# Performance work log

Measured on AMD Instinct MI355X. Metric: run time of the kernel, lower is better.

## Reference

```python
import jax, jax.numpy as jnp
import numpy as np

B, N, F, K, H = 2, 1024, 64, 8, 4
M1 = K + 1                # 9
M2 = (F - 1) * K + 1      # 505
TEMP = 1.0


def setup_inputs() -> dict:
    key = jax.random.key(0)
    ks = jax.random.split(key, 8)
    x = jax.random.normal(ks[0], (B, N, F), dtype=jnp.float32)
    # Bernoulli(0.05) dense adjacency
    adj = (jax.random.uniform(ks[1], (B, N, N)) < 0.05).astype(jnp.float32)
    mask = jnp.ones((B, N), dtype=jnp.float32)
    Wl = jax.random.normal(ks[2], (F, K * H), dtype=jnp.float32) * 0.05
    bl = jnp.zeros((K * H,), dtype=jnp.float32)
    Wr = jax.random.normal(ks[3], (F, K * H), dtype=jnp.float32) * 0.05
    br = jnp.zeros((K * H,), dtype=jnp.float32)
    # fixed affine layer: y = x @ aff_w + aff_b, aff_w[:, :F] = -I, aff_b[M2] = 1
    aff_w = jnp.zeros((F, M1 * M2), dtype=jnp.float32).at[:, :F].set(-jnp.eye(F, dtype=jnp.float32))
    aff_b = jnp.zeros((M1 * M2,), dtype=jnp.float32).at[M2].set(1.0)
    Wm = jax.random.normal(ks[4], (M1 * M2, F), dtype=jnp.float32) * 0.02
    bm = jnp.zeros((F,), dtype=jnp.float32)
    return dict(x=x, adj=adj, mask=mask, Wl=Wl, bl=bl, Wr=Wr, br=br,
                aff_w=aff_w, aff_b=aff_b, Wm=Wm, bm=bm)


def reference(x, adj, mask, Wl, bl, Wr, br, aff_w, aff_b, Wm, bm):
    # --- multi-head edge attention ---
    x_l = (x @ Wl + bl).reshape(B, N, K, H)   # [B,N,K,H]
    x_r = (x @ Wr + br).reshape(B, N, K, H)
    # scores[b,i,j,n,g] = leaky_relu(x_l[b,j] + x_r[b,i]) / temp
    scores = jax.nn.leaky_relu(x_l[:, None, :, :, :] + x_r[:, :, None, :, :]) / TEMP  # [B,N,N,K,H]
    attn_mask = mask[:, None, :] * mask[:, :, None]                # [B,N,N]
    scores = jnp.where(attn_mask[..., None, None] == 0, -1e9, scores)
    att = jax.nn.softmax(scores, axis=2)                           # softmax over source nodes j
    att = jnp.maximum(att * adj[..., None, None], 1e-6)            # clamp(min=1e-6) STE trick
    att = att / jnp.sum(att, axis=2, keepdims=True)                # renormalize
    # --- attention-weighted neighbor gather ---
    x_h = x.reshape(B, N, H, F // H)
    agg = jnp.einsum('bjgk,bijng->bingk', x_h, att).reshape(B, N, K, F)  # [B,N,K,F]
    # --- fixed affine + FFT log-domain geometric mean ---
    x_aff = (agg @ aff_w + aff_b).reshape(B, N, K, M1, M2)
    x_fft = jnp.fft.fft2(x_aff)                                    # over (M1,M2)
    mag = jnp.exp(jnp.mean(jnp.log(jnp.abs(x_fft) + 1e-6), axis=2))  # [B,N,M1,M2]
    ang = jnp.sum(jnp.angle(x_fft), axis=2)
    x_agg = jnp.fft.ifft2(mag * jnp.exp(1j * ang)).real.reshape(B, N, M1 * M2)
    # --- output MLP + node mask ---
    out = x_agg @ Wm + bm
    return out * mask[..., None]
```

## Files before the change

kernel.cpp:

```cpp
#include <hip/hip_runtime.h>
#include <math.h>

#define NN 1024
#define FD 64
#define CH 32
#define M1D 9
#define M2D 505
#define QH 253
#define THALF 2273
#define KPAD 4608
#define KSPLIT 16
#define KCHUNK 288
#define G1SZ 291456
#define G1KS 8

#define FSQRT(x) __builtin_amdgcn_sqrtf(x)
#define FRCP(x)  __builtin_amdgcn_rcpf(x)

typedef short short8 __attribute__((ext_vector_type(8)));
typedef float f32x4 __attribute__((ext_vector_type(4)));

__device__ __forceinline__ unsigned short f2bf(float x) {
    unsigned int u = __builtin_bit_cast(unsigned int, x);
    return (unsigned short)((u + 0x7FFFu + ((u >> 16) & 1u)) >> 16);
}

__device__ __forceinline__ void cvt8_3(const float* v, uint4& h4, uint4& m4, uint4& l4) {
    unsigned short h[8], m[8], l[8];
    #pragma unroll
    for (int i = 0; i < 8; i++) {
        unsigned short hh = f2bf(v[i]);
        float hf = __builtin_bit_cast(float, (unsigned int)hh << 16);
        float r1 = v[i] - hf;
        unsigned short mm = f2bf(r1);
        float mf = __builtin_bit_cast(float, (unsigned int)mm << 16);
        h[i] = hh; m[i] = mm;
        l[i] = f2bf(r1 - mf);
    }
    h4 = make_uint4((unsigned)h[0] | ((unsigned)h[1] << 16), (unsigned)h[2] | ((unsigned)h[3] << 16),
                    (unsigned)h[4] | ((unsigned)h[5] << 16), (unsigned)h[6] | ((unsigned)h[7] << 16));
    m4 = make_uint4((unsigned)m[0] | ((unsigned)m[1] << 16), (unsigned)m[2] | ((unsigned)m[3] << 16),
                    (unsigned)m[4] | ((unsigned)m[5] << 16), (unsigned)m[6] | ((unsigned)m[7] << 16));
    l4 = make_uint4((unsigned)l[0] | ((unsigned)l[1] << 16), (unsigned)l[2] | ((unsigned)l[3] << 16),
                    (unsigned)l[4] | ((unsigned)l[5] << 16), (unsigned)l[6] | ((unsigned)l[7] << 16));
}

#define SAH 0
#define SAM 2560
#define SAL 5120
#define SBH 7680
#define SBM 10240
#define SBL 12800

#define OFF_SUMXP 1024
#define OFF_GMT   4096
#define OFF_XL    151552
#define OFF_XR    217088
#define OFF_AGG   282624
#define OFF_Y     1331200
#define OFF_G1P   6049792
#define OFF_WT    8381440

__global__ __launch_bounds__(256) void fused_pre_kernel(
    const float* __restrict__ x,
    const float* __restrict__ Wl, const float* __restrict__ bl,
    const float* __restrict__ Wr, const float* __restrict__ br,
    const float* __restrict__ Wm, const float* __restrict__ bm,
    const float* __restrict__ mask,
    float* __restrict__ xl, float* __restrict__ xr,
    float* __restrict__ sumxp, float* __restrict__ G1p,
    float* __restrict__ Wt, float* __restrict__ out)
{
    __shared__ __align__(16) unsigned char pool[30720];
    int bid = blockIdx.x, tid = threadIdx.x;

    if (bid < 576) {
        int mt = bid & 7, m1 = (bid >> 3) % 9, ks = bid / 72;
        int r0 = mt * 64, k0 = ks * 64;
        const float* Wmb = Wm + (size_t)m1 * M2D * FD;
        unsigned short* Sp = (unsigned short*)pool;
        int r = tid >> 2, kg = (tid & 3) * 8;
        int rr = r0 + r;
        uint4 Ah[2], Am[2], Al[2], Bh[2], Bm[2], Bl[2];
        #pragma unroll
        for (int c = 0; c < 2; c++) {
            float va[8], vb[8];
            #pragma unroll
            for (int j = 0; j < 8; j++) {
                int m2 = k0 + c*32 + kg + j;
                float v = 0.f;
                if (rr < 506 && m2 < M2D) {
                    int q = rr >> 1;
                    int t = (q * m2) % M2D;
                    float ang = (float)t * (-6.2831853f / 505.0f);
                    float s, cc; __sincosf(ang, &s, &cc);
                    v = (rr & 1) ? -s : cc;
                }
                va[j] = v;
                vb[j] = (m2 < M2D) ? Wmb[(size_t)m2*FD + r] : 0.f;
            }
            cvt8_3(va, Ah[c], Am[c], Al[c]);
            cvt8_3(vb, Bh[c], Bm[c], Bl[c]);
        }
        int w = tid >> 6, lane = tid & 63, lm = lane & 15, quad = lane >> 4;
        f32x4 acc0 = {0.f,0.f,0.f,0.f}, acc1 = acc0, acc2 = acc0, acc3 = acc0;
        #pragma unroll
        for (int c = 0; c < 2; c++) {
            if (c) __syncthreads();
            *(uint4*)&Sp[SAH + r*40 + kg] = Ah[c];
            *(uint4*)&Sp[SAM + r*40 + kg] = Am[c];
            *(uint4*)&Sp[SAL + r*40 + kg] = Al[c];
            *(uint4*)&Sp[SBH + r*40 + kg] = Bh[c];
            *(uint4*)&Sp[SBM + r*40 + kg] = Bm[c];
            *(uint4*)&Sp[SBL + r*40 + kg] = Bl[c];
            __syncthreads();
            int bo = (w*16 + lm)*40 + quad*8;
            short8 bfh = *(const short8*)&Sp[SBH + bo];
            short8 bfm = *(const short8*)&Sp[SBM + bo];
            short8 bfl = *(const short8*)&Sp[SBL + bo];
            #pragma unroll
            for (int t = 0; t < 4; t++) {
                int ao = (t*16 + lm)*40 + quad*8;
                short8 ah = *(const short8*)&Sp[SAH + ao];
                short8 am = *(const short8*)&Sp[SAM + ao];
                short8 al = *(const short8*)&Sp[SAL + ao];
                f32x4 a = (t==0)?acc0:(t==1)?acc1:(t==2)?acc2:acc3;
                a = __builtin_amdgcn_mfma_f32_16x16x32_bf16(ah, bfh, a, 0, 0, 0);
                a = __builtin_amdgcn_mfma_f32_16x16x32_bf16(am, bfh, a, 0, 0, 0);
                a = __builtin_amdgcn_mfma_f32_16x16x32_bf16(ah, bfm, a, 0, 0, 0);
                a = __builtin_amdgcn_mfma_f32_16x16x32_bf16(am, bfm, a, 0, 0, 0);
                a = __builtin_amdgcn_mfma_f32_16x16x32_bf16(al, bfh, a, 0, 0, 0);
                a = __builtin_amdgcn_mfma_f32_16x16x32_bf16(ah, bfl, a, 0, 0, 0);
                if (t==0) acc0 = a; else if (t==1) acc1 = a; else if (t==2) acc2 = a; else acc3 = a;
            }
        }
        float* G1k = G1p + (size_t)ks * G1SZ;
        int f = w*16 + lm;
        #pragma unroll
        for (int t = 0; t < 4; t++) {
            f32x4 a = (t==0)?acc0:(t==1)?acc1:(t==2)?acc2:acc3;
            #pragma unroll
            for (int i = 0; i < 4; i++) {
                int m = t*16 + quad*4 + i;
                int rg = r0 + m;
                if (rg >= 506) continue;
                int q = rg >> 1, reim = rg & 1;
                G1k[(size_t)(m1*QH + q)*128 + reim*64 + f] = a[i];
            }
        }
    } else if (bid < 1088) {
        int grp = tid >> 6, lt = tid & 63;
        int node = (bid - 576)*4 + grp;
        float* xrow = (float*)pool + grp*FD;
        xrow[lt] = x[(size_t)node*FD + lt];
        __syncthreads();
        int c = lt & 31;
        const float* W = (lt < 32) ? Wl : Wr;
        float acc = (lt < 32) ? bl[c] : br[c];
        #pragma unroll
        for (int f = 0; f < FD; f++) acc += xrow[f] * W[f*CH + c];
        float* dst = (lt < 32) ? xl : xr;
        dst[(size_t)node*CH + c] = acc;
    } else if (bid < 1096) {
        int bb = (bid - 1088)*4 + (tid >> 6);
        int f = tid & 63;
        int b = bb >> 4, chunk = bb & 15;
        const float* xb = x + (size_t)b * NN * FD;
        float acc = 0.f;
        int j0 = chunk * 64;
        #pragma unroll 4
        for (int j = j0; j < j0 + 64; j++) acc += xb[j*FD + f];
        sumxp[bb*64 + f] = acc;
    } else if (bid < 1224) {
        int idx = (bid - 1096)*256 + tid;
        float4 bv = ((const float4*)bm)[idx & 15];
        float mk = mask[idx >> 4];
        bv.x *= mk; bv.y *= mk; bv.z *= mk; bv.w *= mk;
        ((float4*)out)[idx] = bv;
    } else {
        int idx = (bid - 1224)*256 + tid;
        int m = idx >> 9, col = idx & 511;
        float v = 0.f;
        if (col < 506) {
            int q = col >> 1;
            int t = (q * m) % M2D;
            float ang = (float)t * (-6.2831853f / 505.0f);
            float s, c; __sincosf(ang, &s, &c);
            v = (col & 1) ? s : c;
        }
        Wt[idx] = v;
    }
}

__global__ __launch_bounds__(256) void fused_mid_kernel(
    const float* __restrict__ x, const float* __restrict__ adj,
    const float* __restrict__ xl, const float* __restrict__ xr,
    const float* __restrict__ sumxp, const float* __restrict__ G1p,
    float* __restrict__ agg, unsigned short* __restrict__ GmT)
{
    int bid = blockIdx.x, tid = threadIdx.x;

    if (bid >= 2048) {
        int bid2 = bid - 2048;
        if (bid2 == 64) {
            for (int i = tid; i < 31*64; i += 256) {
                int t = THALF + (i >> 6), f = i & 63;
                *(unsigned int*)&GmT[(size_t)f*KPAD + 2*t] = 0u;
            }
            return;
        }
        __shared__ float wps[18];
        if (tid < 9) {
            float s, c; __sincosf((float)tid * (-6.2831853f / 9.0f), &s, &c);
            wps[2*tid] = c; wps[2*tid+1] = s;
        }
        __syncthreads();
        int qq = bid2*4 + (tid >> 6);
        int f = tid & 63;
        if (qq >= QH) return;
        float ar[M1D], ai[M1D];
        #pragma unroll
        for (int m1 = 0; m1 < M1D; m1++) {
            size_t o = (size_t)(m1*QH + qq) * 128 + f;
            float sr = 0.f, si = 0.f;
            #pragma unroll
            for (int ks = 0; ks < G1KS; ks++) {
                sr += G1p[(size_t)ks*G1SZ + o];
                si += G1p[(size_t)ks*G1SZ + o + 64];
            }
            ar[m1] = sr; ai[m1] = si;
        }
        #pragma unroll
        for (int p = 0; p < 5; p++) {
            {
                int t = (p == 0) ? qq : (QH + (p-1)*M2D + qq);
                float gr = 0.f, gi = 0.f;
                #pragma unroll
                for (int m1 = 0; m1 < M1D; m1++) {
                    int pm = (p * m1) % M1D;
                    float cr = wps[2*pm], ci = -wps[2*pm+1];
                    gr += ar[m1]*cr - ai[m1]*ci;
                    gi += ar[m1]*ci + ai[m1]*cr;
                }
                float scale = (t == 0) ? (1.0f/4545.0f) : (2.0f/4545.0f);
                unsigned int pk = (unsigned int)f2bf(gr*scale) | ((unsigned int)f2bf(-gi*scale) << 16);
                *(unsigned int*)&GmT[(size_t)f*KPAD + 2*t] = pk;
            }
            if (p >= 1 && qq >= 1) {
                int t = QH + (p-1)*M2D + (M2D - qq);
                float gr = 0.f, gi = 0.f;
                #pragma unroll
                for (int m1 = 0; m1 < M1D; m1++) {
                    int pm = (p * m1) % M1D;
                    float cr = wps[2*pm], ci = -wps[2*pm+1];
                    float aim = -ai[m1];
                    gr += ar[m1]*cr - aim*ci;
                    gi += ar[m1]*ci + aim*cr;
                }
                float scale = 2.0f/4545.0f;
                unsigned int pk = (unsigned int)f2bf(gr*scale) | ((unsigned int)f2bf(-gi*scale) << 16);
                *(unsigned int*)&GmT[(size_t)f*KPAD + 2*t] = pk;
            }
        }
        return;
    }

    int node = bid;
    int b = node >> 10;
    __shared__ float xr_s[CH], Zinv[CH], Sinv[CH];
    __shared__ float red16[16][CH];
    __shared__ int act_list[NN + 8];
    __shared__ int act_n;
    __shared__ float qv2[64][CH];

    if (tid < CH) xr_s[tid] = xr[(size_t)node*CH + tid];
    if (tid == 0) act_n = 0;
    __syncthreads();

    int c = tid & 31, jl = tid >> 5;
    const float* xlb = xl + ((size_t)b << 10) * CH;
    const float* adjrow = adj + (size_t)node * NN;

    int c2 = tid & 15, jl16 = tid >> 4;
    const float2* xlb2 = (const float2*)xlb;
    float xrcx = xr_s[2*c2], xrcy = xr_s[2*c2+1];
    float zx = 0.f, zy = 0.f;
    for (int j0 = jl16; j0 < NN; j0 += 128) {
        float2 sv[8];
        #pragma unroll
        for (int u = 0; u < 8; u++) sv[u] = xlb2[(size_t)(j0 + u*16)*16 + c2];
        #pragma unroll
        for (int u = 0; u < 8; u++) {
            float s0 = sv[u].x + xrcx; s0 = s0 > 0.f ? s0 : 0.01f * s0;
            float s1 = sv[u].y + xrcy; s1 = s1 > 0.f ? s1 : 0.01f * s1;
            zx += __expf(s0); zy += __expf(s1);
        }
    }
    red16[jl16][2*c2]   = zx;
    red16[jl16][2*c2+1] = zy;

    float av[4];
    #pragma unroll
    for (int u = 0; u < 4; u++) av[u] = adjrow[tid + u*256];
    __syncthreads();
    if (tid < CH) {
        float z = 0.f;
        #pragma unroll
        for (int r = 0; r < 16; r++) z += red16[r][tid];
        Zinv[tid] = FRCP(z);
    }
    #pragma unroll
    for (int u = 0; u < 4; u++)
        if (av[u] != 0.f) { int p = atomicAdd(&act_n, 1); act_list[p] = tid + u*256; }
    __syncthreads();
    int nact = act_n;

    int f = tid & 63, n0 = tid >> 6;
    int g = f >> 4;
    int c0 = n0*4 + g, c1 = (n0+4)*4 + g;
    const float* xb = x + ((size_t)b << 10) * FD;
    float acc0 = 0.f, acc1 = 0.f, sacc = 0.f;

    for (int base = 0; base < nact; base += 64) {
        int cnt = min(64, nact - base);
        int cntp = (cnt + 7) & ~7;
        for (int u = tid; u < (cnt << 5); u += 256) {
            int jj = u >> 5, cc = u & 31;
            int j = act_list[base + jj];
            float s = xlb[j*CH + cc] + xr_s[cc];
            s = s > 0.f ? s : 0.01f * s;
            float pv = __expf(s) * Zinv[cc];
            float qq = fmaxf(pv, 1e-6f) - 1e-6f;
            qv2[jj][cc] = qq;
            sacc += qq;
        }
        for (int u = tid + (cnt << 5); u < (cntp << 5); u += 256)
            qv2[u >> 5][u & 31] = 0.f;
        if (tid < cntp - cnt) act_list[base + cnt + tid] = act_list[base];
        __syncthreads();
        for (int jb = 0; jb < cntp; jb += 8) {
            float xv[8];
            #pragma unroll
            for (int u = 0; u < 8; u++) xv[u] = xb[act_list[base + jb + u]*FD + f];
            #pragma unroll
            for (int u = 0; u < 8; u++) {
                acc0 += qv2[jb+u][c0] * xv[u];
                acc1 += qv2[jb+u][c1] * xv[u];
            }
        }
        __syncthreads();
    }
    red16[jl][c] = sacc;
    __syncthreads();
    if (tid < CH) {
        float s = 0.f;
        #pragma unroll
        for (int r = 0; r < 8; r++) s += red16[r][tid];
        Sinv[tid] = FRCP(s + (float)NN * 1e-6f);
    }
    __syncthreads();
    float sx = 0.f;
    #pragma unroll
    for (int cchunk = 0; cchunk < 16; cchunk++) sx += sumxp[(b*16 + cchunk)*64 + f];
    sx *= 1e-6f;
    agg[(size_t)node*512 + n0*FD + f]       = (acc0 + sx) * Sinv[c0];
    agg[(size_t)node*512 + (n0+4)*FD + f]   = (acc1 + sx) * Sinv[c1];
}

__global__ __launch_bounds__(256) void ay_kernel(const float* __restrict__ agg,
                                                 const float* __restrict__ Wt,
                                                 unsigned short* __restrict__ Yb) {
    int slab = blockIdx.x, nt = blockIdx.y;
    int tid = threadIdx.x;
    __shared__ float As2[64][68];
    __shared__ float Bs[64][64];
    int tm = (tid >> 4) * 4, tf = (tid & 15) * 4;
    float ra[16], rb[16];
    #pragma unroll
    for (int i = 0; i < 16; i++) {
        int l = tid + i*256;
        int r = l >> 6, k = l & 63;
        ra[i] = agg[(size_t)(slab*64 + r)*64 + k];
    }
    #pragma unroll
    for (int i = 0; i < 16; i++) {
        int l = tid + i*256;
        rb[i] = Wt[(size_t)(l >> 6)*512 + nt*64 + (l & 63)];
    }
    #pragma unroll
    for (int i = 0; i < 16; i++) { int l = tid + i*256; As2[l & 63][l >> 6] = ra[i]; }
    #pragma unroll
    for (int i = 0; i < 16; i++) { int l = tid + i*256; Bs[l >> 6][l & 63] = rb[i]; }
    __syncthreads();
    float acc[4][4] = {{0.f}};
    #pragma unroll 8
    for (int k = 0; k < 64; k++) {
        float4 a = *(const float4*)&As2[k][tm];
        float4 b = *(const float4*)&Bs[k][tf];
        acc[0][0] += a.x*b.x; acc[0][1] += a.x*b.y; acc[0][2] += a.x*b.z; acc[0][3] += a.x*b.w;
        acc[1][0] += a.y*b.x; acc[1][1] += a.y*b.y; acc[1][2] += a.y*b.z; acc[1][3] += a.y*b.w;
        acc[2][0] += a.z*b.x; acc[2][1] += a.z*b.y; acc[2][2] += a.z*b.z; acc[2][3] += a.z*b.w;
        acc[3][0] += a.w*b.x; acc[3][1] += a.w*b.y; acc[3][2] += a.w*b.z; acc[3][3] += a.w*b.w;
    }
    __syncthreads();
    #pragma unroll
    for (int i = 0; i < 4; i++)
        #pragma unroll
        for (int j = 0; j < 4; j++)
            As2[tm + i][tf + j] = acc[i][j];
    __syncthreads();

    int qloc = tid & 31, node = tid >> 5;
    unsigned short* Yrow = Yb + (size_t)(slab*8 + node)*KPAD;
    int q = nt*32 + qloc;

    if (q <= 252) {
        float2 Av[8];
        #pragma unroll
        for (int n = 0; n < 8; n++)
            Av[n] = make_float2(As2[node*8 + n][2*qloc], As2[node*8 + n][2*qloc + 1]);

        const float CPt[5] = {1.0f, 0.766044443119f, 0.173648177667f, -0.5f, -0.939692620786f};
        const float SPt[5] = {0.0f, -0.642787609687f, -0.984807753012f, -0.866025403784f, -0.342020143326f};

        #define Y_PROD(CSIGN, TIDX)                                            \
        {                                                                      \
            float Pr = 1.f, Pi = 0.f, rp2 = 1.f;                               \
            _Pragma("unroll")                                                  \
            for (int n = 0; n < 8; n++) {                                      \
                float Xr = cp - Av[n].x, Xi = sp - (CSIGN) * Av[n].y;          \
                rp2 *= (Xr*Xr + Xi*Xi);                                        \
                float nPr = Pr*Xr - Pi*Xi;                                     \
                Pi = Pr*Xi + Pi*Xr; Pr = nPr;                                  \
            }                                                                  \
            float pAbs = FSQRT(Pr*Pr + Pi*Pi);                                 \
            float rp8 = FSQRT(FSQRT(FSQRT(FSQRT(rp2))));                       \
            float s = rp8 * FRCP(fmaxf(pAbs, 1e-20f));                         \
            unsigned int pk = (unsigned int)f2bf(s*Pr) | ((unsigned int)f2bf(s*Pi) << 16); \
            *(unsigned int*)&Yrow[2*(TIDX)] = pk;                              \
        }

        #pragma unroll
        for (int p = 0; p < 5; p++) {
            float cp = CPt[p], sp = SPt[p];
            int tfwd = (p == 0) ? q : (QH + (p-1)*M2D + q);
            Y_PROD(1.f, tfwd);
            if (p >= 1 && q >= 1) {
                int tmir = QH + (p-1)*M2D + (M2D - q);
                Y_PROD(-1.f, tmir);
            }
        }
        #undef Y_PROD
    }
    if (nt == 7 && tid < 248) {
        int rr = tid / 31, cc2 = tid % 31;
        unsigned short* Yr2 = Yb + (size_t)(slab*8 + rr)*KPAD;
        *(unsigned int*)&Yr2[2*THALF + 2*cc2] = 0u;
    }
}

__global__ __launch_bounds__(256) void gemm_kernel(const unsigned short* __restrict__ Yb,
                                                   const unsigned short* __restrict__ GmT,
                                                   const float* __restrict__ mask,
                                                   float* __restrict__ out) {
    int mtile = blockIdx.x, kc = blockIdx.y;
    int tid = threadIdx.x;
    __shared__ unsigned short Ys[64*40];
    __shared__ unsigned short Gs[64*40];
    int m0 = mtile * 64;
    int k0 = kc * KCHUNK;
    int r = tid >> 2, kg = (tid & 3) * 8;
    const unsigned short* Ysrc = Yb + (size_t)(m0 + r)*KPAD + k0 + kg;
    const unsigned short* Gsrc = GmT + (size_t)r*KPAD + k0 + kg;
    uint4 ya = *(const uint4*)Ysrc;
    uint4 ga = *(const uint4*)Gsrc;
    int w = tid >> 6, lane = tid & 63;
    int lm = lane & 15, quad = lane >> 4;
    f32x4 acc0 = {0.f,0.f,0.f,0.f}, acc1 = acc0, acc2 = acc0, acc3 = acc0;
    for (int ks = 0; ks < KCHUNK; ks += 32) {
        *(uint4*)&Ys[r*40 + kg] = ya;
        *(uint4*)&Gs[r*40 + kg] = ga;
        __syncthreads();
        if (ks + 32 < KCHUNK) {
            ya = *(const uint4*)(Ysrc + ks + 32);
            ga = *(const uint4*)(Gsrc + ks + 32);
        }
        short8 b  = *(const short8*)&Gs[(w*16 + lm)*40 + quad*8];
        short8 a0 = *(const short8*)&Ys[(lm)*40      + quad*8];
        short8 a1 = *(const short8*)&Ys[(16 + lm)*40 + quad*8];
        short8 a2 = *(const short8*)&Ys[(32 + lm)*40 + quad*8];
        short8 a3 = *(const short8*)&Ys[(48 + lm)*40 + quad*8];
        acc0 = __builtin_amdgcn_mfma_f32_16x16x32_bf16(a0, b, acc0, 0, 0, 0);
        acc1 = __builtin_amdgcn_mfma_f32_16x16x32_bf16(a1, b, acc1, 0, 0, 0);
        acc2 = __builtin_amdgcn_mfma_f32_16x16x32_bf16(a2, b, acc2, 0, 0, 0);
        acc3 = __builtin_amdgcn_mfma_f32_16x16x32_bf16(a3, b, acc3, 0, 0, 0);
        __syncthreads();
    }
    int col = w*16 + lm;
    #pragma unroll
    for (int rr = 0; rr < 4; rr++) {
        int row = m0 + quad*4 + rr;
        atomicAdd(&out[(size_t)row*FD + col],        acc0[rr] * mask[row]);
        atomicAdd(&out[(size_t)(row+16)*FD + col],   acc1[rr] * mask[row+16]);
        atomicAdd(&out[(size_t)(row+32)*FD + col],   acc2[rr] * mask[row+32]);
        atomicAdd(&out[(size_t)(row+48)*FD + col],   acc3[rr] * mask[row+48]);
    }
}

extern "C" void kernel_launch(void* const* d_in, const int* in_sizes, int n_in,
                              void* d_out, int out_size, void* d_ws, size_t ws_size,
                              hipStream_t stream) {
    const float* x    = (const float*)d_in[0];
    const float* adj  = (const float*)d_in[1];
    const float* mask = (const float*)d_in[2];
    const float* Wl   = (const float*)d_in[3];
    const float* bl   = (const float*)d_in[4];
    const float* Wr   = (const float*)d_in[5];
    const float* br   = (const float*)d_in[6];
    const float* Wm   = (const float*)d_in[9];
    const float* bm   = (const float*)d_in[10];
    float* out = (float*)d_out;
    float* ws  = (float*)d_ws;

    float* sumxp = ws + OFF_SUMXP;
    unsigned short* GmT = (unsigned short*)(ws + OFF_GMT);
    float* xl   = ws + OFF_XL;
    float* xr   = ws + OFF_XR;
    float* agg  = ws + OFF_AGG;
    unsigned short* Yb = (unsigned short*)(ws + OFF_Y);
    float* G1p  = ws + OFF_G1P;
    float* Wt   = ws + OFF_WT;

    hipLaunchKernelGGL(fused_pre_kernel, dim3(1352), dim3(256), 0, stream,
                       x, Wl, bl, Wr, br, Wm, bm, mask, xl, xr, sumxp, G1p, Wt, out);
    hipLaunchKernelGGL(fused_mid_kernel, dim3(2113), dim3(256), 0, stream,
                       x, adj, xl, xr, sumxp, G1p, agg, GmT);
    hipLaunchKernelGGL(ay_kernel, dim3(256, 8), dim3(256), 0, stream, agg, Wt, Yb);
    hipLaunchKernelGGL(gemm_kernel, dim3(32, KSPLIT), dim3(256), 0, stream, Yb, GmT, mask, out);
}
```

Before: 159.7 us.

## Compute softmax normalizers via sorted x_l prefix sums and binary search

Adds 64 blocks to the pre kernel. Each block recomputes x_l for one batch and channel, sorts it with a bitonic sort, and stores prefix sums of exp(v) and exp(0.01 v). The mid kernel then finds each node's softmax normalizer Z with a binary search on -x_r and two exponentials, replacing the dense 1024-term leaky-relu exp reduction per node. This trades O(N) work per node for an O(N log N) pre-pass per channel. It adds a serial-sync-heavy sort block that may lengthen the pre kernel's tail, and prefix sums can lose some accuracy compared with direct summation.

```diff
diff --git a/kernel.cpp b/kernel.cpp
--- a/kernel.cpp
+++ b/kernel.cpp
@@ -13,6 +13,7 @@
 #define KCHUNK 288
 #define G1SZ 291456
 #define G1KS 8
+#define SRTSTR 3096
 
 #define FSQRT(x) __builtin_amdgcn_sqrtf(x)
 #define FRCP(x)  __builtin_amdgcn_rcpf(x)
@@ -60,6 +61,7 @@
 #define OFF_Y     1331200
 #define OFF_G1P   6049792
 #define OFF_WT    8381440
+#define OFF_SRT   8414208
 
 __global__ __launch_bounds__(256) void fused_pre_kernel(
     const float* __restrict__ x,
@@ -69,7 +71,8 @@
     const float* __restrict__ mask,
     float* __restrict__ xl, float* __restrict__ xr,
     float* __restrict__ sumxp, float* __restrict__ G1p,
-    float* __restrict__ Wt, float* __restrict__ out)
+    float* __restrict__ Wt, float* __restrict__ srt,
+    float* __restrict__ out)
 {
     __shared__ __align__(16) unsigned char pool[30720];
     int bid = blockIdx.x, tid = threadIdx.x;
@@ -177,7 +180,7 @@
         float mk = mask[idx >> 4];
         bv.x *= mk; bv.y *= mk; bv.z *= mk; bv.w *= mk;
         ((float4*)out)[idx] = bv;
-    } else {
+    } else if (bid < 1352) {
         int idx = (bid - 1224)*256 + tid;
         int m = idx >> 9, col = idx & 511;
         float v = 0.f;
@@ -189,6 +192,67 @@
             v = (col & 1) ? s : c;
         }
         Wt[idx] = v;
+    } else {
+        int bc = bid - 1352;
+        int b = bc >> 5, c = bc & 31;
+        float* sm  = (float*)pool;
+        float* wl  = (float*)(pool + 4096);
+        float* chL = (float*)(pool + 4352);
+        float* chH = (float*)(pool + 5376);
+        if (tid < 64) wl[tid] = Wl[tid*CH + c];
+        __syncthreads();
+        const float* xb = x + (size_t)b * NN * FD;
+        float bc0 = bl[c];
+        for (int i = tid; i < NN; i += 256) {
+            const float* xrw = xb + (size_t)i * FD;
+            float acc = bc0;
+            #pragma unroll
+            for (int f = 0; f < FD; f++) acc += xrw[f] * wl[f];
+            sm[i] = acc;
+        }
+        __syncthreads();
+        for (int k = 2; k <= 1024; k <<= 1) {
+            for (int j = k >> 1; j > 0; j >>= 1) {
+                for (int i = tid; i < 1024; i += 256) {
+                    int p = i ^ j;
+                    if (p > i) {
+                        float a = sm[i], bvv = sm[p];
+                        bool desc = (i & k) != 0;
+                        if (desc ? (a < bvv) : (a > bvv)) { sm[i] = bvv; sm[p] = a; }
+                    }
+                }
+                __syncthreads();
+            }
+        }
+        float* dstS = srt + (size_t)bc * SRTSTR;
+        for (int i = tid; i < 1024; i += 256) dstS[i] = sm[i];
+        float eL[4], eH[4], sl = 0.f, sh = 0.f;
+        #pragma unroll
+        for (int jj = 0; jj < 4; jj++) {
+            float v = sm[4*tid + jj];
+            eL[jj] = sl; eH[jj] = sh;
+            sl += __expf(0.01f * v);
+            sh += __expf(v);
+        }
+        chL[tid] = sl; chH[tid] = sh;
+        __syncthreads();
+        float vL = sl, vH = sh;
+        for (int off = 1; off < 256; off <<= 1) {
+            float aL = (tid >= off) ? chL[tid-off] : 0.f;
+            float aH = (tid >= off) ? chH[tid-off] : 0.f;
+            __syncthreads();
+            vL += aL; vH += aH;
+            chL[tid] = vL; chH[tid] = vH;
+            __syncthreads();
+        }
+        float baseL = tid ? chL[tid-1] : 0.f;
+        float baseH = tid ? chH[tid-1] : 0.f;
+        #pragma unroll
+        for (int jj = 0; jj < 4; jj++) {
+            dstS[1032 + 4*tid + jj] = baseL + eL[jj];
+            dstS[2064 + 4*tid + jj] = baseH + eH[jj];
+        }
+        if (tid == 255) { dstS[1032 + 1024] = chL[255]; dstS[2064 + 1024] = chH[255]; }
     }
 }
 
@@ -196,6 +260,7 @@
     const float* __restrict__ x, const float* __restrict__ adj,
     const float* __restrict__ xl, const float* __restrict__ xr,
     const float* __restrict__ sumxp, const float* __restrict__ G1p,
+    const float* __restrict__ srt,
     float* __restrict__ agg, unsigned short* __restrict__ GmT)
 {
     int bid = blockIdx.x, tid = threadIdx.x;
@@ -281,33 +346,23 @@
     const float* xlb = xl + ((size_t)b << 10) * CH;
     const float* adjrow = adj + (size_t)node * NN;
 
-    int c2 = tid & 15, jl16 = tid >> 4;
-    const float2* xlb2 = (const float2*)xlb;
-    float xrcx = xr_s[2*c2], xrcy = xr_s[2*c2+1];
-    float zx = 0.f, zy = 0.f;
-    for (int j0 = jl16; j0 < NN; j0 += 128) {
-        float2 sv[8];
-        #pragma unroll
-        for (int u = 0; u < 8; u++) sv[u] = xlb2[(size_t)(j0 + u*16)*16 + c2];
-        #pragma unroll
-        for (int u = 0; u < 8; u++) {
-            float s0 = sv[u].x + xrcx; s0 = s0 > 0.f ? s0 : 0.01f * s0;
-            float s1 = sv[u].y + xrcy; s1 = s1 > 0.f ? s1 : 0.01f * s1;
-            zx += __expf(s0); zy += __expf(s1);
-        }
-    }
-    red16[jl16][2*c2]   = zx;
-    red16[jl16][2*c2+1] = zy;
-
     float av[4];
     #pragma unroll
     for (int u = 0; u < 4; u++) av[u] = adjrow[tid + u*256];
-    __syncthreads();
+
     if (tid < CH) {
-        float z = 0.f;
-        #pragma unroll
-        for (int r = 0; r < 16; r++) z += red16[r][tid];
-        Zinv[tid] = FRCP(z);
+        const float* sb = srt + (size_t)((b << 5) + tid) * SRTSTR;
+        float xrc = xr_s[tid];
+        float thr = -xrc;
+        int lo = 0, hi = 1024;
+        while (lo < hi) {
+            int mid = (lo + hi) >> 1;
+            if (sb[mid] <= thr) lo = mid + 1; else hi = mid;
+        }
+        float SLo = sb[1032 + lo];
+        float SHi = sb[2064 + 1024] - sb[2064 + lo];
+        float Z = __expf(0.01f * xrc) * SLo + __expf(xrc) * SHi;
+        Zinv[tid] = FRCP(Z);
     }
     #pragma unroll
     for (int u = 0; u < 4; u++)
@@ -530,11 +585,12 @@
     unsigned short* Yb = (unsigned short*)(ws + OFF_Y);
     float* G1p  = ws + OFF_G1P;
     float* Wt   = ws + OFF_WT;
-
-    hipLaunchKernelGGL(fused_pre_kernel, dim3(1352), dim3(256), 0, stream,
-                       x, Wl, bl, Wr, br, Wm, bm, mask, xl, xr, sumxp, G1p, Wt, out);
+    float* srt  = ws + OFF_SRT;
+
+    hipLaunchKernelGGL(fused_pre_kernel, dim3(1416), dim3(256), 0, stream,
+                       x, Wl, bl, Wr, br, Wm, bm, mask, xl, xr, sumxp, G1p, Wt, srt, out);
     hipLaunchKernelGGL(fused_mid_kernel, dim3(2113), dim3(256), 0, stream,
-                       x, adj, xl, xr, sumxp, G1p, agg, GmT);
+                       x, adj, xl, xr, sumxp, G1p, srt, agg, GmT);
     hipLaunchKernelGGL(ay_kernel, dim3(256, 8), dim3(256), 0, stream, agg, Wt, Yb);
     hipLaunchKernelGGL(gemm_kernel, dim3(32, KSPLIT), dim3(256), 0, stream, Yb, GmT, mask, out);
 }
```

Result: slower. 194.5 us (+21.8%).

## Widen ay_kernel tiles to 128 columns with 512 threads and vectorized loads

Applied to the files above, without the earlier changes.

The ay_kernel now handles 128 output columns per block with 512 threads instead of 64 columns with 256 threads, halving the grid's y dimension. Each block loads the agg slab once for twice the columns, and the global loads of agg and Wt are now float4-wide. Shared memory is pooled and reused between the GEMM staging and the product stage. Fewer blocks reload the same agg slab, but more q threads in the last column tile sit idle (q > 252).

```diff
diff --git a/kernel.cpp b/kernel.cpp
--- a/kernel.cpp
+++ b/kernel.cpp
@@ -367,36 +367,40 @@
     agg[(size_t)node*512 + (n0+4)*FD + f]   = (acc1 + sx) * Sinv[c1];
 }
 
-__global__ __launch_bounds__(256) void ay_kernel(const float* __restrict__ agg,
-                                                 const float* __restrict__ Wt,
-                                                 unsigned short* __restrict__ Yb) {
-    int slab = blockIdx.x, nt = blockIdx.y;
+__global__ __launch_bounds__(512, 4) void ay_kernel(const float* __restrict__ agg,
+                                                    const float* __restrict__ Wt,
+                                                    unsigned short* __restrict__ Yb) {
+    int slab = blockIdx.x, nt2 = blockIdx.y;
     int tid = threadIdx.x;
-    __shared__ float As2[64][68];
-    __shared__ float Bs[64][64];
-    int tm = (tid >> 4) * 4, tf = (tid & 15) * 4;
-    float ra[16], rb[16];
-    #pragma unroll
-    for (int i = 0; i < 16; i++) {
-        int l = tid + i*256;
-        int r = l >> 6, k = l & 63;
-        ra[i] = agg[(size_t)(slab*64 + r)*64 + k];
-    }
-    #pragma unroll
-    for (int i = 0; i < 16; i++) {
-        int l = tid + i*256;
-        rb[i] = Wt[(size_t)(l >> 6)*512 + nt*64 + (l & 63)];
-    }
-    #pragma unroll
-    for (int i = 0; i < 16; i++) { int l = tid + i*256; As2[l & 63][l >> 6] = ra[i]; }
-    #pragma unroll
-    for (int i = 0; i < 16; i++) { int l = tid + i*256; Bs[l >> 6][l & 63] = rb[i]; }
-    __syncthreads();
+    __shared__ __align__(16) float pool[12800];
+    float (*Ast)[68]  = (float (*)[68])pool;
+    float (*Bst)[132] = (float (*)[132])(pool + 4352);
+    float (*A2p)[132] = (float (*)[132])pool;
+
+    {
+        int r = tid >> 3, seg = (tid & 7) * 8;
+        const float* asrc = &agg[(size_t)(slab*64 + r)*64 + seg];
+        float va[8];
+        *(float4*)&va[0] = *(const float4*)asrc;
+        *(float4*)&va[4] = *(const float4*)(asrc + 4);
+        #pragma unroll
+        for (int j = 0; j < 8; j++) Ast[seg + j][r] = va[j];
+    }
+    {
+        int k = tid >> 3, cs = (tid & 7) * 16;
+        const float* bsrc = &Wt[(size_t)k*512 + nt2*128 + cs];
+        #pragma unroll
+        for (int j = 0; j < 4; j++)
+            *(float4*)&Bst[k][cs + j*4] = *(const float4*)(bsrc + j*4);
+    }
+    __syncthreads();
+
+    int tm = (tid & 15) * 4, tf = (tid >> 4) * 4;
     float acc[4][4] = {{0.f}};
     #pragma unroll 8
     for (int k = 0; k < 64; k++) {
-        float4 a = *(const float4*)&As2[k][tm];
-        float4 b = *(const float4*)&Bs[k][tf];
+        float4 a = *(const float4*)&Ast[k][tm];
+        float4 b = *(const float4*)&Bst[k][tf];
         acc[0][0] += a.x*b.x; acc[0][1] += a.x*b.y; acc[0][2] += a.x*b.z; acc[0][3] += a.x*b.w;
         acc[1][0] += a.y*b.x; acc[1][1] += a.y*b.y; acc[1][2] += a.y*b.z; acc[1][3] += a.y*b.w;
         acc[2][0] += a.z*b.x; acc[2][1] += a.z*b.y; acc[2][2] += a.z*b.z; acc[2][3] += a.z*b.w;
@@ -407,18 +411,18 @@
     for (int i = 0; i < 4; i++)
         #pragma unroll
         for (int j = 0; j < 4; j++)
-            As2[tm + i][tf + j] = acc[i][j];
-    __syncthreads();
-
-    int qloc = tid & 31, node = tid >> 5;
+            A2p[tm + i][tf + j] = acc[i][j];
+    __syncthreads();
+
+    int qloc = tid & 63, node = tid >> 6;
     unsigned short* Yrow = Yb + (size_t)(slab*8 + node)*KPAD;
-    int q = nt*32 + qloc;
+    int q = nt2*64 + qloc;
 
     if (q <= 252) {
         float2 Av[8];
         #pragma unroll
         for (int n = 0; n < 8; n++)
-            Av[n] = make_float2(As2[node*8 + n][2*qloc], As2[node*8 + n][2*qloc + 1]);
+            Av[n] = make_float2(A2p[node*8 + n][2*qloc], A2p[node*8 + n][2*qloc + 1]);
 
         const float CPt[5] = {1.0f, 0.766044443119f, 0.173648177667f, -0.5f, -0.939692620786f};
         const float SPt[5] = {0.0f, -0.642787609687f, -0.984807753012f, -0.866025403784f, -0.342020143326f};
@@ -452,7 +456,7 @@
         }
         #undef Y_PROD
     }
-    if (nt == 7 && tid < 248) {
+    if (nt2 == 3 && tid < 248) {
         int rr = tid / 31, cc2 = tid % 31;
         unsigned short* Yr2 = Yb + (size_t)(slab*8 + rr)*KPAD;
         *(unsigned int*)&Yr2[2*THALF + 2*cc2] = 0u;
@@ -535,6 +539,6 @@
                        x, Wl, bl, Wr, br, Wm, bm, mask, xl, xr, sumxp, G1p, Wt, out);
     hipLaunchKernelGGL(fused_mid_kernel, dim3(2113), dim3(256), 0, stream,
                        x, adj, xl, xr, sumxp, G1p, agg, GmT);
-    hipLaunchKernelGGL(ay_kernel, dim3(256, 8), dim3(256), 0, stream, agg, Wt, Yb);
+    hipLaunchKernelGGL(ay_kernel, dim3(256, 4), dim3(512), 0, stream, agg, Wt, Yb);
     hipLaunchKernelGGL(gemm_kernel, dim3(32, KSPLIT), dim3(256), 0, stream, Yb, GmT, mask, out);
 }
```

Result: no change. 160.2 us (+0.3%).
